# Optimization experiments

Measured on AMD Instinct MI355X. Metric: run time of the kernel, lower is better.

## Reference

```python
import jax, jax.numpy as jnp
import numpy as np

B, N, C, H, EXP = 8, 1024, 256, 8, 4
D = C // H
F = int(C * EXP * 2 / 3)  # 682, GLU hidden size
EPS = 1e-3  # keras LayerNormalization default


def layer_norm(x, g, b):
    m = jnp.mean(x, axis=-1, keepdims=True)
    v = jnp.mean(jnp.square(x - m), axis=-1, keepdims=True)
    return (x - m) * jax.lax.rsqrt(v + EPS) * g + b


def setup_inputs() -> dict:
    key = jax.random.key(0)
    ks = jax.random.split(key, 16)
    inputs = jax.random.normal(ks[0], (B, N, C), jnp.float32)
    # ragged padding mask: random valid lengths per batch element
    lengths = jax.random.randint(ks[1], (B,), N // 2, N + 1)
    valid = jnp.arange(N)[None, :] < lengths[:, None]          # [B,N]
    mask = valid[:, :, None] & valid[:, None, :]               # [B,N,N]
    interaction = jax.random.normal(ks[2], (B, N, N, H), jnp.float32)
    s = lambda k, sh, fan: jax.random.normal(k, sh, jnp.float32) / np.sqrt(fan)
    return {
        "inputs": inputs, "mask": mask, "interaction": interaction,
        "Wqkv": s(ks[3], (C, 3 * C), C), "bqkv": jnp.zeros((3 * C,), jnp.float32),
        "Wt1": s(ks[4], (H, H), H), "bt1": jnp.zeros((H,), jnp.float32),
        "Wt2": s(ks[5], (H, H), H), "bt2": jnp.zeros((H,), jnp.float32),
        "Wout": s(ks[6], (C, C), C), "bout": jnp.zeros((C,), jnp.float32),
        "ln1_g": jnp.ones((C,), jnp.float32), "ln1_b": jnp.zeros((C,), jnp.float32),
        "ln2_g": jnp.ones((C,), jnp.float32), "ln2_b": jnp.zeros((C,), jnp.float32),
        "gamma1": jnp.full((C,), 1e-5, jnp.float32),
        "gamma2": jnp.full((C,), 1e-5, jnp.float32),
        "W_wide": s(ks[7], (C, F), C), "W_gate": s(ks[8], (C, F), C),
        "W_down": s(ks[9], (F, C), F),
        "lnf_g": jnp.ones((F,), jnp.float32), "lnf_b": jnp.zeros((F,), jnp.float32),
    }


def reference(inputs, mask, interaction, Wqkv, bqkv, Wt1, bt1, Wt2, bt2,
              Wout, bout, ln1_g, ln1_b, ln2_g, ln2_b, gamma1, gamma2,
              W_wide, W_gate, W_down, lnf_g, lnf_b):
    # --- pre-norm talking-heads self-attention ---
    h = layer_norm(inputs, ln1_g, ln1_b)
    qkv = (h @ Wqkv + bqkv).reshape(B, N, 3, H, D)
    qkv = jnp.transpose(qkv, (2, 0, 3, 1, 4))                 # [3,B,H,N,D]
    q, k, v = qkv[0], qkv[1], qkv[2]
    scores = jnp.einsum('bhnd,bhmd->bhnm', q, k) / np.sqrt(D) # [B,H,N,N]
    # talking heads 1 (pre-softmax head mixing, with bias)
    scores = jnp.einsum('bhnm,hg->bgnm', scores, Wt1) + bt1[None, :, None, None]
    scores = scores + jnp.transpose(interaction, (0, 3, 1, 2))
    # keras Softmax(mask): add -1e9 to masked positions
    scores = jnp.where(mask[:, None, :, :], scores, scores - 1e9)
    attn = jax.nn.softmax(scores, axis=-1)                    # pure attention
    # talking heads 2 (post-softmax head mixing)
    attn2 = jnp.einsum('bhnm,hg->bgnm', attn, Wt2) + bt2[None, :, None, None]
    out = jnp.einsum('bhnm,bhmd->bhnd', attn2, v)
    out = jnp.transpose(out, (0, 2, 1, 3)).reshape(B, N, C)
    out = out @ Wout + bout
    x = inputs + gamma1 * out                                  # LayerScale residual
    # --- GLU FFN with inner LayerNorm ---
    h2 = layer_norm(x, ln2_g, ln2_b)
    f = jax.nn.gelu(h2 @ W_wide, approximate=False) * (h2 @ W_gate)
    f = layer_norm(f, lnf_g, lnf_b)
    f = f @ W_down
    x = x + gamma2 * f
    return x
```

## Files before the change

kernel.cpp:

```cpp
#include <hip/hip_runtime.h>
#include <hip/hip_bf16.h>
#include <math.h>

#define B_ 8
#define N_ 1024
#define C_ 256
#define H_ 8
#define D_ 32
#define F_ 682
#define FP_ 704
#define EPS_ 1e-3f

typedef const __hip_bfloat16* bf16cp;
typedef __hip_bfloat16 bf16;
typedef __attribute__((ext_vector_type(8))) short short8;
typedef __attribute__((ext_vector_type(4))) float f32x4;

__device__ __forceinline__ float b2f(bf16 v){ return __bfloat162float(v); }
__device__ __forceinline__ float us2f(unsigned int u){ return __uint_as_float(u << 16); }
__device__ __forceinline__ unsigned short f2bu(float f){
  unsigned int u = __float_as_uint(f);
  return (unsigned short)((u + 0x7FFFu + ((u >> 16) & 1u)) >> 16);
}

__device__ __forceinline__ float ldf(const void* p, size_t i, int bf){
  return bf ? b2f(((bf16cp)p)[i]) : ((const float*)p)[i];
}

struct Ptrs { const void* p[22]; };

__global__ void k_sniff(Ptrs ptrs, int* flags){
  if (threadIdx.x != 0 || blockIdx.x != 0) return;
  const int sizes[22] = {2097152, 8388608, 8388608, 196608, 768, 64, 8, 64, 8,
                         65536, 256, 256, 256, 256, 256, 256, 256,
                         174592, 174592, 174592, 682, 682};
  for (int i = 0; i < 22; i++){
    if (i == 1){ flags[i] = 0; continue; }
    const unsigned short* u = (const unsigned short*)ptrs.p[i];
    int nu = sizes[i] < 64 ? sizes[i] : 64;
    int badB = 0, badF = 0, evenAllZero = 1, oddAny = 0;
    for (int j = 0; j < nu; j++){
      unsigned short x = u[j];
      float vb = us2f((unsigned int)x);
      float ab = fabsf(vb);
      if (!(vb == 0.0f) && (!(ab <= 1e3f) || ab < 1e-30f || vb != vb)) badB++;
      if ((j & 1) == 0){ if (x) evenAllZero = 0; }
      else            { if (x) oddAny = 1; }
    }
    for (int j = 0; j + 1 < nu; j += 2){
      unsigned int w = ((unsigned int)u[j]) | (((unsigned int)u[j+1]) << 16);
      float vf = __uint_as_float(w);
      float af = fabsf(vf);
      if (!(vf == 0.0f) && (!(af <= 1e3f) || af < 1e-30f || vf != vf)) badF++;
    }
    int bf;
    if (badB > badF) bf = 0;
    else if (badF > badB) bf = 1;
    else bf = (evenAllZero && oddAny) ? 0 : 1;
    flags[i] = bf;
  }
}

__global__ __launch_bounds__(256) void k_lengths(const unsigned char* mask, int* lengths){
  __shared__ int red[256];
  int b = blockIdx.x, t = threadIdx.x;
  unsigned char c0 = mask[0], c1 = mask[1];
  int mode;
  if (c0 == 0x80u) mode = 2;
  else if (c0 == 0u) mode = 3;
  else mode = (c1 != 0u) ? 0 : 1;
  int cnt = 0;
  for (int n = t; n < N_; n += 256){
    size_t idx = ((size_t)b*N_ + n)*N_ + n;
    int v;
    if (mode == 0)      v = (mask[idx] != 0);
    else if (mode == 1) v = (((const int*)mask)[idx] != 0);
    else if (mode == 2) v = (((const unsigned short*)mask)[idx] != 0);
    else                v = (((const float*)mask)[idx] != 0.0f);
    cnt += v;
  }
  red[t] = cnt; __syncthreads();
  for (int s = 128; s > 0; s >>= 1){ if (t < s) red[t] += red[t+s]; __syncthreads(); }
  if (t == 0) lengths[b] = red[0];
}

__global__ __launch_bounds__(256) void k_ln(const void* in, const int* flags, int in_mode,
                                            const void* g, int gi, const void* bia, int bi,
                                            void* out, int out_bf16, int Clen, int stride){
  __shared__ float red[256];
  int fin = (in_mode >= 0) ? flags[in_mode] : (in_mode == -2 ? 1 : 0);
  int fg = flags[gi], fb = flags[bi];
  int row = blockIdx.x, t = threadIdx.x;
  size_t base = (size_t)row * stride;
  float xs[3];
  int nv = (Clen + 255) >> 8;
  float s = 0.f;
  for (int i = 0; i < nv; i++){
    int c = t + (i << 8);
    float v = 0.f;
    if (c < Clen) v = ldf(in, base+c, fin);
    xs[i] = v; s += v;
  }
  red[t] = s; __syncthreads();
  for (int st = 128; st > 0; st >>= 1){ if (t < st) red[t] += red[t+st]; __syncthreads(); }
  float mean = red[0] / (float)Clen; __syncthreads();
  float s2 = 0.f;
  for (int i = 0; i < nv; i++){
    int c = t + (i << 8);
    if (c < Clen){ float d = xs[i] - mean; s2 += d*d; }
  }
  red[t] = s2; __syncthreads();
  for (int st = 128; st > 0; st >>= 1){ if (t < st) red[t] += red[t+st]; __syncthreads(); }
  float rstd = rsqrtf(red[0] / (float)Clen + EPS_);
  for (int i = 0; i < nv; i++){
    int c = t + (i << 8);
    if (c < Clen){
      float v = (xs[i]-mean)*rstd*ldf(g,c,fg) + ldf(bia,c,fb);
      if (out_bf16) ((bf16*)out)[base+c] = __float2bfloat16(v);
      else          ((float*)out)[base+c] = v;
    }
  }
}

__global__ __launch_bounds__(256) void k_prepw(Ptrs ptrs, const int* flags,
                                               unsigned short* wqkvT, unsigned short* woutT,
                                               unsigned short* wwideT, unsigned short* wgateT,
                                               unsigned short* wdownT){
  __shared__ unsigned short tile[32][33];
  int which = blockIdx.y;
  const void* src; unsigned short* dst; int f, Ksrc, Nsrc, Np, Kp;
  switch (which){
    case 0:  src = ptrs.p[3];  f = flags[3];  Ksrc = 256; Nsrc = 768; Np = 768; Kp = 256; dst = wqkvT; break;
    case 1:  src = ptrs.p[9];  f = flags[9];  Ksrc = 256; Nsrc = 256; Np = 256; Kp = 256; dst = woutT; break;
    case 2:  src = ptrs.p[17]; f = flags[17]; Ksrc = 256; Nsrc = F_;  Np = FP_; Kp = 256; dst = wwideT; break;
    case 3:  src = ptrs.p[18]; f = flags[18]; Ksrc = 256; Nsrc = F_;  Np = FP_; Kp = 256; dst = wgateT; break;
    default: src = ptrs.p[19]; f = flags[19]; Ksrc = F_;  Nsrc = 256; Np = 256; Kp = FP_; dst = wdownT; break;
  }
  int tilesN = (Np + 31) >> 5, tilesK = (Kp + 31) >> 5;
  int tid = blockIdx.x;
  if (tid >= tilesN * tilesK) return;
  int tn = tid % tilesN, tk = tid / tilesN;
  int n0 = tn << 5, k0 = tk << 5;
  int tx = threadIdx.x & 31, ty = threadIdx.x >> 5;
  #pragma unroll
  for (int i = 0; i < 4; i++){
    int k = k0 + ty + i*8, n = n0 + tx;
    float v = (k < Ksrc && n < Nsrc) ? ldf(src, (size_t)k*Nsrc + n, f) : 0.f;
    tile[ty + i*8][tx] = f2bu(v);
  }
  __syncthreads();
  #pragma unroll
  for (int i = 0; i < 4; i++){
    int n = n0 + ty + i*8, k = k0 + tx;
    if (n < Np && k < Kp) dst[(size_t)n*Kp + k] = tile[tx][ty + i*8];
  }
}

__device__ __forceinline__ void gemm128_core(const unsigned short* A, const unsigned short* BT,
                                             int K, int m0, int n0,
                                             unsigned short* As, unsigned short* Bs,
                                             f32x4 (&acc)[4][4]){
  int t = threadIdx.x;
  int lane = t & 63, w = t >> 6, wr = w >> 1, wc = w & 1;
  int cl = lane & 15, cq = lane >> 4;
  int r0 = t >> 2, o0 = (t & 3) << 3;
  const unsigned short* Ap = A + (size_t)(m0 + r0) * K + o0;
  const unsigned short* Bp = BT + (size_t)(n0 + r0) * K + o0;
  for (int k0 = 0; k0 < K; k0 += 32){
    short8 a0 = *(const short8*)(Ap + k0);
    short8 a1 = *(const short8*)(Ap + (size_t)64*K + k0);
    short8 b0 = *(const short8*)(Bp + k0);
    short8 b1 = *(const short8*)(Bp + (size_t)64*K + k0);
    __syncthreads();
    *(short8*)(As + r0*40 + o0)      = a0;
    *(short8*)(As + (r0+64)*40 + o0) = a1;
    *(short8*)(Bs + r0*40 + o0)      = b0;
    *(short8*)(Bs + (r0+64)*40 + o0) = b1;
    __syncthreads();
    short8 af[4], bfr[4];
    #pragma unroll
    for (int i = 0; i < 4; i++){
      af[i]  = *(const short8*)(As + (wr*64 + i*16 + cl)*40 + cq*8);
      bfr[i] = *(const short8*)(Bs + (wc*64 + i*16 + cl)*40 + cq*8);
    }
    #pragma unroll
    for (int i = 0; i < 4; i++)
      #pragma unroll
      for (int j = 0; j < 4; j++)
        acc[i][j] = __builtin_amdgcn_mfma_f32_16x16x32_bf16(af[i], bfr[j], acc[i][j], 0, 0, 0);
  }
}

__global__ __launch_bounds__(256) void k_qkv(const bf16* Abuf, const unsigned short* WT,
                                             const void* bias, const int* flags,
                                             bf16* qb, bf16* kb, bf16* vb){
  __shared__ unsigned short As[128*40], Bs[128*40];
  int fb = flags[4];
  int m0 = blockIdx.x * 128, n0 = blockIdx.y * 128;
  f32x4 acc[4][4];
  #pragma unroll
  for (int i = 0; i < 4; i++)
    #pragma unroll
    for (int j = 0; j < 4; j++){ f32x4 z = {0.f,0.f,0.f,0.f}; acc[i][j] = z; }
  gemm128_core((const unsigned short*)Abuf, WT, C_, m0, n0, As, Bs, acc);
  int t = threadIdx.x, lane = t & 63, w = t >> 6, wr = w >> 1, wc = w & 1;
  int cl = lane & 15, cq = lane >> 4;
  #pragma unroll
  for (int j = 0; j < 4; j++){
    int n = n0 + wc*64 + j*16 + cl;
    float bv = ldf(bias, n, fb);
    int three = n >> 8, hh = (n >> 5) & 7, d = n & 31;
    bf16* dst = (three == 0) ? qb : ((three == 1) ? kb : vb);
    #pragma unroll
    for (int i = 0; i < 4; i++){
      #pragma unroll
      for (int r = 0; r < 4; r++){
        int m = m0 + wr*64 + i*16 + cq*4 + r;
        int bb = m >> 10, nn = m & 1023;
        dst[(((size_t)bb*H_ + hh)*N_ + nn)*D_ + d] = __float2bfloat16(acc[i][j][r] + bv);
      }
    }
  }
}

__global__ __launch_bounds__(256) void k_outproj(const bf16* Abuf, const unsigned short* WT,
                                                 const void* bias, const void* inputs,
                                                 const void* gamma1, const int* flags, float* xout){
  __shared__ unsigned short As[128*40], Bs[128*40];
  int fb = flags[10], fin = flags[0], fg = flags[15];
  int m0 = blockIdx.x * 128, n0 = blockIdx.y * 128;
  f32x4 acc[4][4];
  #pragma unroll
  for (int i = 0; i < 4; i++)
    #pragma unroll
    for (int j = 0; j < 4; j++){ f32x4 z = {0.f,0.f,0.f,0.f}; acc[i][j] = z; }
  gemm128_core((const unsigned short*)Abuf, WT, C_, m0, n0, As, Bs, acc);
  int t = threadIdx.x, lane = t & 63, w = t >> 6, wr = w >> 1, wc = w & 1;
  int cl = lane & 15, cq = lane >> 4;
  #pragma unroll
  for (int j = 0; j < 4; j++){
    int n = n0 + wc*64 + j*16 + cl;
    float bv = ldf(bias, n, fb);
    float gv = ldf(gamma1, n, fg);
    #pragma unroll
    for (int i = 0; i < 4; i++){
      #pragma unroll
      for (int r = 0; r < 4; r++){
        int m = m0 + wr*64 + i*16 + cq*4 + r;
        size_t idx = (size_t)m*C_ + n;
        xout[idx] = ldf(inputs, idx, fin) + gv * (acc[i][j][r] + bv);
      }
    }
  }
}

__device__ __forceinline__ float gelu_exact(float x){
  return 0.5f * x * (1.0f + erff(x * 0.70710678118654752f));
}

__global__ __launch_bounds__(256) void k_ffn1(const bf16* Abuf, const unsigned short* WwT,
                                              const unsigned short* WgT, bf16* fout){
  __shared__ unsigned short As[128*40], Bw[64*40], Bg[64*40];
  int m0 = blockIdx.x * 128, n0 = blockIdx.y * 64;
  int t = threadIdx.x, lane = t & 63, w = t >> 6, wr = w >> 1, wc = w & 1;
  int cl = lane & 15, cq = lane >> 4;
  int r0 = t >> 2, o0 = (t & 3) << 3;
  const unsigned short* A = (const unsigned short*)Abuf;
  f32x4 acc1[4][2], acc2[4][2];
  #pragma unroll
  for (int i = 0; i < 4; i++)
    #pragma unroll
    for (int j = 0; j < 2; j++){ f32x4 z = {0.f,0.f,0.f,0.f}; acc1[i][j] = z; acc2[i][j] = z; }
  const unsigned short* Ap = A + (size_t)(m0 + r0) * C_ + o0;
  const unsigned short* Bwp = WwT + (size_t)(n0 + r0) * C_ + o0;
  const unsigned short* Bgp = WgT + (size_t)(n0 + r0) * C_ + o0;
  for (int k0 = 0; k0 < C_; k0 += 32){
    short8 a0 = *(const short8*)(Ap + k0);
    short8 a1 = *(const short8*)(Ap + (size_t)64*C_ + k0);
    short8 b0, c0;
    if (r0 < 64){
      b0 = *(const short8*)(Bwp + k0);
      c0 = *(const short8*)(Bgp + k0);
    }
    __syncthreads();
    *(short8*)(As + r0*40 + o0)      = a0;
    *(short8*)(As + (r0+64)*40 + o0) = a1;
    if (r0 < 64){
      *(short8*)(Bw + r0*40 + o0) = b0;
      *(short8*)(Bg + r0*40 + o0) = c0;
    }
    __syncthreads();
    short8 af[4], bfr[2], cfr[2];
    #pragma unroll
    for (int i = 0; i < 4; i++)
      af[i] = *(const short8*)(As + (wr*64 + i*16 + cl)*40 + cq*8);
    #pragma unroll
    for (int j = 0; j < 2; j++){
      bfr[j] = *(const short8*)(Bw + (wc*32 + j*16 + cl)*40 + cq*8);
      cfr[j] = *(const short8*)(Bg + (wc*32 + j*16 + cl)*40 + cq*8);
    }
    #pragma unroll
    for (int i = 0; i < 4; i++)
      #pragma unroll
      for (int j = 0; j < 2; j++){
        acc1[i][j] = __builtin_amdgcn_mfma_f32_16x16x32_bf16(af[i], bfr[j], acc1[i][j], 0, 0, 0);
        acc2[i][j] = __builtin_amdgcn_mfma_f32_16x16x32_bf16(af[i], cfr[j], acc2[i][j], 0, 0, 0);
      }
  }
  #pragma unroll
  for (int j = 0; j < 2; j++){
    int n = n0 + wc*32 + j*16 + cl;
    #pragma unroll
    for (int i = 0; i < 4; i++){
      #pragma unroll
      for (int r = 0; r < 4; r++){
        int m = m0 + wr*64 + i*16 + cq*4 + r;
        float v = (n < F_) ? gelu_exact(acc1[i][j][r]) * acc2[i][j][r] : 0.f;
        fout[(size_t)m*FP_ + n] = __float2bfloat16(v);
      }
    }
  }
}

__global__ __launch_bounds__(256) void k_down(const bf16* Abuf, const unsigned short* WT,
                                              const float* xbuf, const void* gamma2,
                                              const int* flags, void* out){
  __shared__ unsigned short As[128*40], Bs[128*40];
  int fg = flags[16], fo = flags[0];
  int m0 = blockIdx.x * 128, n0 = blockIdx.y * 128;
  f32x4 acc[4][4];
  #pragma unroll
  for (int i = 0; i < 4; i++)
    #pragma unroll
    for (int j = 0; j < 4; j++){ f32x4 z = {0.f,0.f,0.f,0.f}; acc[i][j] = z; }
  gemm128_core((const unsigned short*)Abuf, WT, FP_, m0, n0, As, Bs, acc);
  int t = threadIdx.x, lane = t & 63, w = t >> 6, wr = w >> 1, wc = w & 1;
  int cl = lane & 15, cq = lane >> 4;
  #pragma unroll
  for (int j = 0; j < 4; j++){
    int n = n0 + wc*64 + j*16 + cl;
    float gv = ldf(gamma2, n, fg);
    #pragma unroll
    for (int i = 0; i < 4; i++){
      #pragma unroll
      for (int r = 0; r < 4; r++){
        int m = m0 + wr*64 + i*16 + cq*4 + r;
        size_t idx = (size_t)m*C_ + n;
        float val = xbuf[idx] + gv * acc[i][j][r];
        if (fo) ((bf16*)out)[idx] = __float2bfloat16(val);
        else    ((float*)out)[idx] = val;
      }
    }
  }
}

__global__ __launch_bounds__(256) void k_vsum(const bf16* vb, float* vsum){
  __shared__ float red[8][32];
  int bg = blockIdx.x;
  int t = threadIdx.x;
  int d = t & 31, mg = t >> 5;
  float s = 0.f;
  for (int m = mg*128; m < mg*128 + 128; m++)
    s += b2f(vb[((size_t)bg*N_ + m)*D_ + d]);
  red[mg][d] = s; __syncthreads();
  if (t < 32){
    float a = 0.f;
    #pragma unroll
    for (int i = 0; i < 8; i++) a += red[i][t];
    vsum[(size_t)bg*D_ + t] = a;
  }
}

__global__ __launch_bounds__(256) void k_stats2(const bf16* qb, const bf16* kb,
                                                const void* Wt1, const void* bt1, const void* inter,
                                                const int* flags, const int* lengths, float2* stats){
  __shared__ float w1s[64], b1v[8];
  __shared__ float swM[4][8][16], swL[4][8][16];
  int fw1 = flags[5], fb1 = flags[6], fint = flags[2];
  int t = threadIdx.x;
  int ntile = blockIdx.x, b = blockIdx.y;
  int n0 = ntile * 16;
  int len = lengths[b];
  if (t < 64) w1s[t] = ldf(Wt1, t, fw1) * 0.17677669529663687f;
  if (t < 8)  b1v[t] = ldf(bt1, t, fb1);
  __syncthreads();
  int lane = t & 63, w = t >> 6;
  int c = lane & 15, q = lane >> 4;
  const unsigned short* qus = (const unsigned short*)qb;
  const unsigned short* kus = (const unsigned short*)kb;
  short8 qfrag[8];
  #pragma unroll
  for (int h = 0; h < 8; h++)
    qfrag[h] = *(const short8*)(qus + (((size_t)b*8 + h)*N_ + n0 + c)*D_ + q*8);
  int n_g = n0 + c;
  float M[8], L[8];
  #pragma unroll
  for (int g = 0; g < 8; g++){ M[g] = -1e30f; L[g] = 0.f; }

  for (int ci = 0; ci < 8; ci++){
    int m0c = w*256 + ci*32;
    #pragma unroll
    for (int mt = 0; mt < 2; mt++){
      int m0t = m0c + mt*16;
      f32x4 sfr[8];
      #pragma unroll
      for (int h = 0; h < 8; h++){
        short8 kf = *(const short8*)(kus + (((size_t)b*8 + h)*N_ + m0t + c)*D_ + q*8);
        f32x4 z = {0.f,0.f,0.f,0.f};
        sfr[h] = __builtin_amdgcn_mfma_f32_16x16x32_bf16(kf, qfrag[h], z, 0, 0, 0);
      }
      float ifl[4][8];
      #pragma unroll
      for (int r = 0; r < 4; r++){
        int m = m0t + q*4 + r;
        size_t i8 = ((size_t)b*N_ + n_g)*N_ + m;
        if (fint){
          uint4 iv = *(const uint4*)((const unsigned short*)inter + i8*8);
          ifl[r][0]=us2f(iv.x&0xffffu); ifl[r][1]=us2f(iv.x>>16);
          ifl[r][2]=us2f(iv.y&0xffffu); ifl[r][3]=us2f(iv.y>>16);
          ifl[r][4]=us2f(iv.z&0xffffu); ifl[r][5]=us2f(iv.z>>16);
          ifl[r][6]=us2f(iv.w&0xffffu); ifl[r][7]=us2f(iv.w>>16);
        } else {
          const float* fp = (const float*)inter + i8*8;
          #pragma unroll
          for (int g = 0; g < 8; g++) ifl[r][g] = fp[g];
        }
      }
      #pragma unroll
      for (int g = 0; g < 8; g++){
        float sv[4];
        #pragma unroll
        for (int r = 0; r < 4; r++){
          int m = m0t + q*4 + r;
          float v = b1v[g] + ifl[r][g];
          #pragma unroll
          for (int h = 0; h < 8; h++) v += sfr[h][r] * w1s[h*8 + g];
          bool ok = (n_g >= len) || (m < len);
          sv[r] = ok ? v : -1e30f;
        }
        float tmax = fmaxf(fmaxf(sv[0], sv[1]), fmaxf(sv[2], sv[3]));
        float Mn = fmaxf(M[g], tmax);
        float f = __expf(M[g] - Mn);
        L[g] = L[g]*f + __expf(sv[0]-Mn) + __expf(sv[1]-Mn) + __expf(sv[2]-Mn) + __expf(sv[3]-Mn);
        M[g] = Mn;
      }
    }
  }
  #pragma unroll
  for (int g = 0; g < 8; g++){
    #pragma unroll
    for (int sft = 16; sft <= 32; sft <<= 1){
      float Mo = __shfl_xor(M[g], sft);
      float Lo = __shfl_xor(L[g], sft);
      float Mn = fmaxf(M[g], Mo);
      L[g] = L[g]*__expf(M[g]-Mn) + Lo*__expf(Mo-Mn);
      M[g] = Mn;
    }
  }
  if (lane < 16){
    #pragma unroll
    for (int g = 0; g < 8; g++){ swM[w][g][c] = M[g]; swL[w][g][c] = L[g]; }
  }
  __syncthreads();
  if (t < 128){
    int g = t >> 4, nl = t & 15;
    float Mf = fmaxf(fmaxf(swM[0][g][nl], swM[1][g][nl]), fmaxf(swM[2][g][nl], swM[3][g][nl]));
    float Lf = 0.f;
    #pragma unroll
    for (int wv = 0; wv < 4; wv++) Lf += swL[wv][g][nl] * __expf(swM[wv][g][nl] - Mf);
    stats[((size_t)b*8 + g)*N_ + n0 + nl] = make_float2(Mf, Lf);
  }
}

__global__ __launch_bounds__(256) void k_attn2(const bf16* qb, const bf16* kb, const bf16* vb,
                                               const void* Wt1, const void* bt1,
                                               const void* Wt2, const void* bt2,
                                               const void* inter, const int* flags,
                                               const int* lengths, const float2* stats,
                                               const float* vsum, bf16* aobuf){
  __shared__ unsigned short a2s[4][8][640];
  __shared__ unsigned short vts[4][1280];
  __shared__ float w1s[64], w2s[64], b1v[8], b2v[8];
  __shared__ float moff[8][16];
  __shared__ float vsumS[8][32];
  __shared__ float osum[4][528];
  int fw1 = flags[5], fb1 = flags[6], fw2 = flags[7], fb2 = flags[8], fint = flags[2];
  int t = threadIdx.x;
  int ntile = blockIdx.x, b = blockIdx.y;
  int n0 = ntile * 16;
  int len = lengths[b];
  if (t < 64){ w1s[t] = ldf(Wt1, t, fw1) * 0.17677669529663687f; w2s[t] = ldf(Wt2, t, fw2); }
  if (t < 8){ b1v[t] = ldf(bt1, t, fb1); b2v[t] = ldf(bt2, t, fb2); }
  if (t < 128){
    int g = t >> 4, nl = t & 15;
    float2 st = stats[((size_t)b*8 + g)*N_ + n0 + nl];
    moff[g][nl] = st.x + __logf(st.y);
  }
  {
    int g = t >> 5, d = t & 31;
    vsumS[g][d] = vsum[((size_t)b*8 + g)*D_ + d];
  }
  __syncthreads();
  int lane = t & 63, w = t >> 6;
  int c = lane & 15, q = lane >> 4;
  const unsigned short* qus = (const unsigned short*)qb;
  const unsigned short* kus = (const unsigned short*)kb;
  const unsigned short* vus = (const unsigned short*)vb;
  short8 qfrag[8];
  #pragma unroll
  for (int h = 0; h < 8; h++)
    qfrag[h] = *(const short8*)(qus + (((size_t)b*8 + h)*N_ + n0 + c)*D_ + q*8);
  float moffreg[8][4];
  #pragma unroll
  for (int g = 0; g < 8; g++)
    #pragma unroll
    for (int r = 0; r < 4; r++) moffreg[g][r] = moff[g][q*4 + r];
  f32x4 acc[8][2];
  #pragma unroll
  for (int gg = 0; gg < 8; gg++){ f32x4 z = {0.f,0.f,0.f,0.f}; acc[gg][0] = z; acc[gg][1] = z; }

  for (int ci = 0; ci < 8; ci++){
    int m0c = w*256 + ci*32;
    #pragma unroll
    for (int mt = 0; mt < 2; mt++){
      int m0t = m0c + mt*16;
      f32x4 sfr[8];
      #pragma unroll
      for (int h = 0; h < 8; h++){
        short8 kf = *(const short8*)(kus + (((size_t)b*8 + h)*N_ + m0t + c)*D_ + q*8);
        f32x4 z = {0.f,0.f,0.f,0.f};
        sfr[h] = __builtin_amdgcn_mfma_f32_16x16x32_bf16(qfrag[h], kf, z, 0, 0, 0);
      }
      int m_g = m0t + c;
      bool mok = (m_g < len);
      #pragma unroll
      for (int r = 0; r < 4; r++){
        int n_l = q*4 + r, n_gg = n0 + n_l;
        size_t i8 = ((size_t)b*N_ + n_gg)*N_ + m_g;
        float ifl[8];
        if (fint){
          uint4 iv = *(const uint4*)((const unsigned short*)inter + i8*8);
          ifl[0]=us2f(iv.x&0xffffu); ifl[1]=us2f(iv.x>>16);
          ifl[2]=us2f(iv.y&0xffffu); ifl[3]=us2f(iv.y>>16);
          ifl[4]=us2f(iv.z&0xffffu); ifl[5]=us2f(iv.z>>16);
          ifl[6]=us2f(iv.w&0xffffu); ifl[7]=us2f(iv.w>>16);
        } else {
          const float* fp = (const float*)inter + i8*8;
          #pragma unroll
          for (int g = 0; g < 8; g++) ifl[g] = fp[g];
        }
        bool ok = (n_gg >= len) || mok;
        float p[8];
        #pragma unroll
        for (int g = 0; g < 8; g++){
          float v = b1v[g] + ifl[g];
          #pragma unroll
          for (int h = 0; h < 8; h++) v += sfr[h][r] * w1s[h*8 + g];
          v = ok ? v : -1e30f;
          p[g] = __expf(v - moffreg[g][r]);
        }
        #pragma unroll
        for (int gg = 0; gg < 8; gg++){
          float a2 = 0.f;
          #pragma unroll
          for (int g = 0; g < 8; g++) a2 += p[g] * w2s[g*8 + gg];
          a2s[w][gg][n_l*40 + mt*16 + c] = f2bu(a2);
        }
      }
    }
    #pragma unroll
    for (int gg = 0; gg < 8; gg++){
      short8 v0 = *(const short8*)(vus + (((size_t)b*8 + gg)*N_ + m0c + c)*D_ + q*8);
      short8 v1 = *(const short8*)(vus + (((size_t)b*8 + gg)*N_ + m0c + 16 + c)*D_ + q*8);
      #pragma unroll
      for (int j = 0; j < 8; j++){
        vts[w][(q*8 + j)*40 + c]      = (unsigned short)v0[j];
        vts[w][(q*8 + j)*40 + 16 + c] = (unsigned short)v1[j];
      }
      short8 af  = *(const short8*)&a2s[w][gg][c*40 + q*8];
      short8 bf0 = *(const short8*)&vts[w][c*40 + q*8];
      short8 bf1 = *(const short8*)&vts[w][(16 + c)*40 + q*8];
      acc[gg][0] = __builtin_amdgcn_mfma_f32_16x16x32_bf16(af, bf0, acc[gg][0], 0, 0, 0);
      acc[gg][1] = __builtin_amdgcn_mfma_f32_16x16x32_bf16(af, bf1, acc[gg][1], 0, 0, 0);
    }
  }
  for (int gg = 0; gg < 8; gg++){
    #pragma unroll
    for (int dt = 0; dt < 2; dt++)
      #pragma unroll
      for (int r = 0; r < 4; r++)
        osum[w][(q*4 + r)*33 + dt*16 + c] = acc[gg][dt][r];
    __syncthreads();
    #pragma unroll
    for (int e = t; e < 512; e += 256){
      int nl = e >> 5, d = e & 31;
      float val = osum[0][nl*33 + d] + osum[1][nl*33 + d]
                + osum[2][nl*33 + d] + osum[3][nl*33 + d]
                + b2v[gg] * vsumS[gg][d];
      aobuf[((size_t)b*N_ + n0 + nl)*C_ + gg*D_ + d] = __float2bfloat16(val);
    }
    __syncthreads();
  }
}

extern "C" void kernel_launch(void* const* d_in, const int* in_sizes, int n_in,
                              void* d_out, int out_size, void* d_ws, size_t ws_size,
                              hipStream_t stream) {
  Ptrs ptrs;
  for (int i = 0; i < 22; i++) ptrs.p[i] = d_in[i];
  const unsigned char* mask = (const unsigned char*)d_in[1];

  char* ws = (char*)d_ws;
  size_t o = 0;
  size_t o_flags = o; o += 256;
  size_t o_len   = o; o += 256;
  size_t o_stats = o; o += (size_t)B_*H_*N_*sizeof(float2);
  size_t o_vsum  = o; o += (size_t)B_*H_*D_*4;
  size_t o_h     = o; o += (size_t)B_*N_*C_*2;
  size_t o_q     = o; o += (size_t)B_*N_*C_*2;
  size_t o_k     = o; o += (size_t)B_*N_*C_*2;
  size_t o_v     = o; o += (size_t)B_*N_*C_*2;
  size_t o_ao    = o; o += (size_t)B_*N_*C_*2;
  size_t o_x     = o; o += (size_t)B_*N_*C_*4;
  size_t o_f     = o; o += (size_t)B_*N_*FP_*2;
  size_t o_wq    = o; o += (size_t)768*256*2;
  size_t o_wo    = o; o += (size_t)256*256*2;
  size_t o_ww    = o; o += (size_t)FP_*256*2;
  size_t o_wg    = o; o += (size_t)FP_*256*2;
  size_t o_wd    = o; o += (size_t)256*FP_*2;

  int*    flags   = (int*)(ws + o_flags);
  int*    lengths = (int*)(ws + o_len);
  float2* stats   = (float2*)(ws + o_stats);
  float*  vsum    = (float*)(ws + o_vsum);
  bf16*   hbuf    = (bf16*)(ws + o_h);
  bf16*   qbuf    = (bf16*)(ws + o_q);
  bf16*   kbuf    = (bf16*)(ws + o_k);
  bf16*   vbuf    = (bf16*)(ws + o_v);
  bf16*   aobuf   = (bf16*)(ws + o_ao);
  float*  xbuf    = (float*)(ws + o_x);
  bf16*   fbuf    = (bf16*)(ws + o_f);
  unsigned short* wqkvT  = (unsigned short*)(ws + o_wq);
  unsigned short* woutT  = (unsigned short*)(ws + o_wo);
  unsigned short* wwideT = (unsigned short*)(ws + o_ww);
  unsigned short* wgateT = (unsigned short*)(ws + o_wg);
  unsigned short* wdownT = (unsigned short*)(ws + o_wd);

  k_sniff<<<1, 64, 0, stream>>>(ptrs, flags);
  k_prepw<<<dim3(192, 5), 256, 0, stream>>>(ptrs, flags, wqkvT, woutT, wwideT, wgateT, wdownT);
  k_lengths<<<8, 256, 0, stream>>>(mask, lengths);
  k_ln<<<B_*N_, 256, 0, stream>>>(d_in[0], flags, 0, d_in[11], 11, d_in[12], 12, hbuf, 1, C_, C_);
  k_qkv<<<dim3(64, 6), 256, 0, stream>>>(hbuf, wqkvT, d_in[4], flags, qbuf, kbuf, vbuf);
  k_vsum<<<64, 256, 0, stream>>>(vbuf, vsum);
  k_stats2<<<dim3(64, 8), 256, 0, stream>>>(qbuf, kbuf, d_in[5], d_in[6], d_in[2],
                                            flags, lengths, stats);
  k_attn2<<<dim3(64, 8), 256, 0, stream>>>(qbuf, kbuf, vbuf, d_in[5], d_in[6], d_in[7], d_in[8],
                                           d_in[2], flags, lengths, stats, vsum, aobuf);
  k_outproj<<<dim3(64, 2), 256, 0, stream>>>(aobuf, woutT, d_in[10], d_in[0], d_in[15], flags, xbuf);
  k_ln<<<B_*N_, 256, 0, stream>>>(xbuf, flags, -1, d_in[13], 13, d_in[14], 14, hbuf, 1, C_, C_);
  k_ffn1<<<dim3(64, 11), 256, 0, stream>>>(hbuf, wwideT, wgateT, fbuf);
  k_ln<<<B_*N_, 256, 0, stream>>>(fbuf, flags, -2, d_in[20], 20, d_in[21], 21, fbuf, 1, F_, FP_);
  k_down<<<dim3(64, 2), 256, 0, stream>>>(fbuf, wdownT, xbuf, d_in[16], flags, d_out);
}
```

Measured before the change: 1.024 ms.

## Materialize unnormalized softmax probabilities once and split attention into two passes

The attention is restructured so scores and the interaction tensor are computed only once. Pass A computes the exponentiated scores without max-subtraction, writes them as a bf16 probability buffer of B*H*N*N, and accumulates row sums. Pass B reads that buffer, normalizes it, applies the post-softmax head mix, and multiplies by a pre-transposed V, with heads split over a z grid dimension. This removes the duplicated QK and interaction reads from the old stats-then-attn pair but adds a large 128MB intermediate round trip, and dropping max-subtraction risks exp overflow. The format sniff kernel is also parallelized across blocks with wave ballots.

```diff
diff --git a/kernel.cpp b/kernel.cpp
--- a/kernel.cpp
+++ b/kernel.cpp
@@ -29,30 +29,40 @@
 
 struct Ptrs { const void* p[22]; };
 
-__global__ void k_sniff(Ptrs ptrs, int* flags){
-  if (threadIdx.x != 0 || blockIdx.x != 0) return;
+__global__ __launch_bounds__(64) void k_sniffp(Ptrs ptrs, int* flags){
+  int i = blockIdx.x;
+  int lane = threadIdx.x;
+  if (i == 1){ if (lane == 0) flags[1] = 0; return; }
   const int sizes[22] = {2097152, 8388608, 8388608, 196608, 768, 64, 8, 64, 8,
                          65536, 256, 256, 256, 256, 256, 256, 256,
                          174592, 174592, 174592, 682, 682};
-  for (int i = 0; i < 22; i++){
-    if (i == 1){ flags[i] = 0; continue; }
-    const unsigned short* u = (const unsigned short*)ptrs.p[i];
-    int nu = sizes[i] < 64 ? sizes[i] : 64;
-    int badB = 0, badF = 0, evenAllZero = 1, oddAny = 0;
-    for (int j = 0; j < nu; j++){
-      unsigned short x = u[j];
-      float vb = us2f((unsigned int)x);
-      float ab = fabsf(vb);
-      if (!(vb == 0.0f) && (!(ab <= 1e3f) || ab < 1e-30f || vb != vb)) badB++;
-      if ((j & 1) == 0){ if (x) evenAllZero = 0; }
-      else            { if (x) oddAny = 1; }
-    }
-    for (int j = 0; j + 1 < nu; j += 2){
-      unsigned int w = ((unsigned int)u[j]) | (((unsigned int)u[j+1]) << 16);
-      float vf = __uint_as_float(w);
-      float af = fabsf(vf);
-      if (!(vf == 0.0f) && (!(af <= 1e3f) || af < 1e-30f || vf != vf)) badF++;
-    }
+  const unsigned short* u = (const unsigned short*)ptrs.p[i];
+  int nu = sizes[i] < 64 ? sizes[i] : 64;
+  unsigned short x = 0;
+  if (lane < nu) x = u[lane];
+  int predB = 0;
+  if (lane < nu){
+    float vb = us2f((unsigned int)x);
+    float ab = fabsf(vb);
+    predB = (!(vb == 0.0f) && (!(ab <= 1e3f) || ab < 1e-30f || vb != vb)) ? 1 : 0;
+  }
+  unsigned long long mB = __ballot(predB);
+  int badB = __popcll(mB);
+  unsigned long long mEven = __ballot(lane < nu && (lane & 1) == 0 && x != 0);
+  unsigned long long mOdd  = __ballot(lane < nu && (lane & 1) == 1 && x != 0);
+  int evenAllZero = (mEven == 0ull);
+  int oddAny = (mOdd != 0ull);
+  unsigned short xa = (unsigned short)__shfl((int)x, (lane * 2) & 63);
+  unsigned short xb = (unsigned short)__shfl((int)x, (lane * 2 + 1) & 63);
+  int predF = 0;
+  if (lane < (nu >> 1)){
+    unsigned int w = ((unsigned int)xa) | (((unsigned int)xb) << 16);
+    float vf = __uint_as_float(w);
+    float af = fabsf(vf);
+    predF = (!(vf == 0.0f) && (!(af <= 1e3f) || af < 1e-30f || vf != vf)) ? 1 : 0;
+  }
+  int badF = __popcll(__ballot(predF));
+  if (lane == 0){
     int bf;
     if (badB > badF) bf = 0;
     else if (badF > badB) bf = 1;
@@ -153,6 +163,24 @@
   for (int i = 0; i < 4; i++){
     int n = n0 + ty + i*8, k = k0 + tx;
     if (n < Np && k < Kp) dst[(size_t)n*Kp + k] = tile[tx][ty + i*8];
+  }
+}
+
+__global__ __launch_bounds__(256) void k_vt(const bf16* vb, unsigned short* vt){
+  __shared__ unsigned short tile[32][34];
+  int mt = blockIdx.x, bg = blockIdx.y;
+  int tx = threadIdx.x & 31, ty = threadIdx.x >> 5;
+  const unsigned short* vus = (const unsigned short*)vb;
+  #pragma unroll
+  for (int i = 0; i < 4; i++){
+    int m = mt*32 + ty + i*8;
+    tile[ty + i*8][tx] = vus[((size_t)bg*N_ + m)*D_ + tx];
+  }
+  __syncthreads();
+  #pragma unroll
+  for (int i = 0; i < 4; i++){
+    int d = ty + i*8;
+    vt[((size_t)bg*D_ + d)*N_ + mt*32 + tx] = tile[tx][d];
   }
 }
 
@@ -371,14 +399,16 @@
   }
 }
 
-__global__ __launch_bounds__(256) void k_stats2(const bf16* qb, const bf16* kb,
-                                                const void* Wt1, const void* bt1, const void* inter,
-                                                const int* flags, const int* lengths, float2* stats){
+__global__ __launch_bounds__(256) void k_passA(const bf16* qb, const bf16* kb,
+                                               const void* Wt1, const void* bt1, const void* inter,
+                                               const int* flags, const int* lengths,
+                                               unsigned short* P, float* Lp){
   __shared__ float w1s[64], b1v[8];
-  __shared__ float swM[4][8][16], swL[4][8][16];
+  __shared__ unsigned short ps[4][8][640];
+  __shared__ float swL[4][8][16];
   int fw1 = flags[5], fb1 = flags[6], fint = flags[2];
   int t = threadIdx.x;
-  int ntile = blockIdx.x, b = blockIdx.y;
+  int ntile = blockIdx.x, b = blockIdx.y, z = blockIdx.z;
   int n0 = ntile * 16;
   int len = lengths[b];
   if (t < 64) w1s[t] = ldf(Wt1, t, fw1) * 0.17677669529663687f;
@@ -392,13 +422,14 @@
   #pragma unroll
   for (int h = 0; h < 8; h++)
     qfrag[h] = *(const short8*)(qus + (((size_t)b*8 + h)*N_ + n0 + c)*D_ + q*8);
-  int n_g = n0 + c;
-  float M[8], L[8];
-  #pragma unroll
-  for (int g = 0; g < 8; g++){ M[g] = -1e30f; L[g] = 0.f; }
-
-  for (int ci = 0; ci < 8; ci++){
-    int m0c = w*256 + ci*32;
+  float Lacc[8][4];
+  #pragma unroll
+  for (int g = 0; g < 8; g++)
+    #pragma unroll
+    for (int r = 0; r < 4; r++) Lacc[g][r] = 0.f;
+
+  for (int ci = 0; ci < 4; ci++){
+    int m0c = z*512 + w*128 + ci*32;
     #pragma unroll
     for (int mt = 0; mt < 2; mt++){
       int m0t = m0c + mt*16;
@@ -406,130 +437,8 @@
       #pragma unroll
       for (int h = 0; h < 8; h++){
         short8 kf = *(const short8*)(kus + (((size_t)b*8 + h)*N_ + m0t + c)*D_ + q*8);
-        f32x4 z = {0.f,0.f,0.f,0.f};
-        sfr[h] = __builtin_amdgcn_mfma_f32_16x16x32_bf16(kf, qfrag[h], z, 0, 0, 0);
-      }
-      float ifl[4][8];
-      #pragma unroll
-      for (int r = 0; r < 4; r++){
-        int m = m0t + q*4 + r;
-        size_t i8 = ((size_t)b*N_ + n_g)*N_ + m;
-        if (fint){
-          uint4 iv = *(const uint4*)((const unsigned short*)inter + i8*8);
-          ifl[r][0]=us2f(iv.x&0xffffu); ifl[r][1]=us2f(iv.x>>16);
-          ifl[r][2]=us2f(iv.y&0xffffu); ifl[r][3]=us2f(iv.y>>16);
-          ifl[r][4]=us2f(iv.z&0xffffu); ifl[r][5]=us2f(iv.z>>16);
-          ifl[r][6]=us2f(iv.w&0xffffu); ifl[r][7]=us2f(iv.w>>16);
-        } else {
-          const float* fp = (const float*)inter + i8*8;
-          #pragma unroll
-          for (int g = 0; g < 8; g++) ifl[r][g] = fp[g];
-        }
-      }
-      #pragma unroll
-      for (int g = 0; g < 8; g++){
-        float sv[4];
-        #pragma unroll
-        for (int r = 0; r < 4; r++){
-          int m = m0t + q*4 + r;
-          float v = b1v[g] + ifl[r][g];
-          #pragma unroll
-          for (int h = 0; h < 8; h++) v += sfr[h][r] * w1s[h*8 + g];
-          bool ok = (n_g >= len) || (m < len);
-          sv[r] = ok ? v : -1e30f;
-        }
-        float tmax = fmaxf(fmaxf(sv[0], sv[1]), fmaxf(sv[2], sv[3]));
-        float Mn = fmaxf(M[g], tmax);
-        float f = __expf(M[g] - Mn);
-        L[g] = L[g]*f + __expf(sv[0]-Mn) + __expf(sv[1]-Mn) + __expf(sv[2]-Mn) + __expf(sv[3]-Mn);
-        M[g] = Mn;
-      }
-    }
-  }
-  #pragma unroll
-  for (int g = 0; g < 8; g++){
-    #pragma unroll
-    for (int sft = 16; sft <= 32; sft <<= 1){
-      float Mo = __shfl_xor(M[g], sft);
-      float Lo = __shfl_xor(L[g], sft);
-      float Mn = fmaxf(M[g], Mo);
-      L[g] = L[g]*__expf(M[g]-Mn) + Lo*__expf(Mo-Mn);
-      M[g] = Mn;
-    }
-  }
-  if (lane < 16){
-    #pragma unroll
-    for (int g = 0; g < 8; g++){ swM[w][g][c] = M[g]; swL[w][g][c] = L[g]; }
-  }
-  __syncthreads();
-  if (t < 128){
-    int g = t >> 4, nl = t & 15;
-    float Mf = fmaxf(fmaxf(swM[0][g][nl], swM[1][g][nl]), fmaxf(swM[2][g][nl], swM[3][g][nl]));
-    float Lf = 0.f;
-    #pragma unroll
-    for (int wv = 0; wv < 4; wv++) Lf += swL[wv][g][nl] * __expf(swM[wv][g][nl] - Mf);
-    stats[((size_t)b*8 + g)*N_ + n0 + nl] = make_float2(Mf, Lf);
-  }
-}
-
-__global__ __launch_bounds__(256) void k_attn2(const bf16* qb, const bf16* kb, const bf16* vb,
-                                               const void* Wt1, const void* bt1,
-                                               const void* Wt2, const void* bt2,
-                                               const void* inter, const int* flags,
-                                               const int* lengths, const float2* stats,
-                                               const float* vsum, bf16* aobuf){
-  __shared__ unsigned short a2s[4][8][640];
-  __shared__ unsigned short vts[4][1280];
-  __shared__ float w1s[64], w2s[64], b1v[8], b2v[8];
-  __shared__ float moff[8][16];
-  __shared__ float vsumS[8][32];
-  __shared__ float osum[4][528];
-  int fw1 = flags[5], fb1 = flags[6], fw2 = flags[7], fb2 = flags[8], fint = flags[2];
-  int t = threadIdx.x;
-  int ntile = blockIdx.x, b = blockIdx.y;
-  int n0 = ntile * 16;
-  int len = lengths[b];
-  if (t < 64){ w1s[t] = ldf(Wt1, t, fw1) * 0.17677669529663687f; w2s[t] = ldf(Wt2, t, fw2); }
-  if (t < 8){ b1v[t] = ldf(bt1, t, fb1); b2v[t] = ldf(bt2, t, fb2); }
-  if (t < 128){
-    int g = t >> 4, nl = t & 15;
-    float2 st = stats[((size_t)b*8 + g)*N_ + n0 + nl];
-    moff[g][nl] = st.x + __logf(st.y);
-  }
-  {
-    int g = t >> 5, d = t & 31;
-    vsumS[g][d] = vsum[((size_t)b*8 + g)*D_ + d];
-  }
-  __syncthreads();
-  int lane = t & 63, w = t >> 6;
-  int c = lane & 15, q = lane >> 4;
-  const unsigned short* qus = (const unsigned short*)qb;
-  const unsigned short* kus = (const unsigned short*)kb;
-  const unsigned short* vus = (const unsigned short*)vb;
-  short8 qfrag[8];
-  #pragma unroll
-  for (int h = 0; h < 8; h++)
-    qfrag[h] = *(const short8*)(qus + (((size_t)b*8 + h)*N_ + n0 + c)*D_ + q*8);
-  float moffreg[8][4];
-  #pragma unroll
-  for (int g = 0; g < 8; g++)
-    #pragma unroll
-    for (int r = 0; r < 4; r++) moffreg[g][r] = moff[g][q*4 + r];
-  f32x4 acc[8][2];
-  #pragma unroll
-  for (int gg = 0; gg < 8; gg++){ f32x4 z = {0.f,0.f,0.f,0.f}; acc[gg][0] = z; acc[gg][1] = z; }
-
-  for (int ci = 0; ci < 8; ci++){
-    int m0c = w*256 + ci*32;
-    #pragma unroll
-    for (int mt = 0; mt < 2; mt++){
-      int m0t = m0c + mt*16;
-      f32x4 sfr[8];
-      #pragma unroll
-      for (int h = 0; h < 8; h++){
-        short8 kf = *(const short8*)(kus + (((size_t)b*8 + h)*N_ + m0t + c)*D_ + q*8);
-        f32x4 z = {0.f,0.f,0.f,0.f};
-        sfr[h] = __builtin_amdgcn_mfma_f32_16x16x32_bf16(qfrag[h], kf, z, 0, 0, 0);
+        f32x4 zz = {0.f,0.f,0.f,0.f};
+        sfr[h] = __builtin_amdgcn_mfma_f32_16x16x32_bf16(qfrag[h], kf, zz, 0, 0, 0);
       }
       int m_g = m0t + c;
       bool mok = (m_g < len);
@@ -550,54 +459,136 @@
           for (int g = 0; g < 8; g++) ifl[g] = fp[g];
         }
         bool ok = (n_gg >= len) || mok;
-        float p[8];
         #pragma unroll
         for (int g = 0; g < 8; g++){
           float v = b1v[g] + ifl[g];
           #pragma unroll
           for (int h = 0; h < 8; h++) v += sfr[h][r] * w1s[h*8 + g];
-          v = ok ? v : -1e30f;
-          p[g] = __expf(v - moffreg[g][r]);
+          float e = ok ? __expf(v) : 0.f;
+          Lacc[g][r] += e;
+          ps[w][g][n_l*40 + mt*16 + c] = f2bu(e);
         }
-        #pragma unroll
-        for (int gg = 0; gg < 8; gg++){
-          float a2 = 0.f;
-          #pragma unroll
-          for (int g = 0; g < 8; g++) a2 += p[g] * w2s[g*8 + gg];
-          a2s[w][gg][n_l*40 + mt*16 + c] = f2bu(a2);
-        }
-      }
-    }
-    #pragma unroll
-    for (int gg = 0; gg < 8; gg++){
-      short8 v0 = *(const short8*)(vus + (((size_t)b*8 + gg)*N_ + m0c + c)*D_ + q*8);
-      short8 v1 = *(const short8*)(vus + (((size_t)b*8 + gg)*N_ + m0c + 16 + c)*D_ + q*8);
-      #pragma unroll
-      for (int j = 0; j < 8; j++){
-        vts[w][(q*8 + j)*40 + c]      = (unsigned short)v0[j];
-        vts[w][(q*8 + j)*40 + 16 + c] = (unsigned short)v1[j];
-      }
-      short8 af  = *(const short8*)&a2s[w][gg][c*40 + q*8];
-      short8 bf0 = *(const short8*)&vts[w][c*40 + q*8];
-      short8 bf1 = *(const short8*)&vts[w][(16 + c)*40 + q*8];
+      }
+    }
+    #pragma unroll
+    for (int it = 0; it < 8; it++){
+      int row = it*16 + (lane >> 2);
+      int g = row >> 4, n = row & 15, chunk = lane & 3;
+      short8 pv = *(const short8*)&ps[w][g][n*40 + chunk*8];
+      *(short8*)(P + (((size_t)b*8 + g)*N_ + n0 + n)*N_ + m0c + chunk*8) = pv;
+    }
+  }
+  #pragma unroll
+  for (int g = 0; g < 8; g++)
+    #pragma unroll
+    for (int r = 0; r < 4; r++){
+      float v = Lacc[g][r];
+      v += __shfl_xor(v, 1); v += __shfl_xor(v, 2);
+      v += __shfl_xor(v, 4); v += __shfl_xor(v, 8);
+      Lacc[g][r] = v;
+    }
+  if (c == 0){
+    #pragma unroll
+    for (int g = 0; g < 8; g++)
+      #pragma unroll
+      for (int r = 0; r < 4; r++) swL[w][g][q*4 + r] = Lacc[g][r];
+  }
+  __syncthreads();
+  if (t < 128){
+    int g = t >> 4, nl = t & 15;
+    float Lf = swL[0][g][nl] + swL[1][g][nl] + swL[2][g][nl] + swL[3][g][nl];
+    Lp[(((size_t)b*8 + g)*N_ + n0 + nl)*2 + z] = Lf;
+  }
+}
+
+__global__ __launch_bounds__(256) void k_passB(const unsigned short* P, const unsigned short* vt,
+                                               const void* Wt2, const void* bt2,
+                                               const int* flags, const float* Lp,
+                                               const float* vsum, bf16* aobuf){
+  __shared__ float w2s[64], b2v[8];
+  __shared__ float rLs[8][16];
+  __shared__ float vsumS[4][32];
+  __shared__ float osum[4][528];
+  int fw2 = flags[7], fb2 = flags[8];
+  int t = threadIdx.x;
+  int ntile = blockIdx.x, b = blockIdx.y, zh = blockIdx.z;
+  int n0 = ntile * 16;
+  if (t < 64) w2s[t] = ldf(Wt2, t, fw2);
+  if (t < 8)  b2v[t] = ldf(bt2, t, fb2);
+  if (t < 128){
+    int g = t >> 4, nl = t & 15;
+    const float* lp = Lp + (((size_t)b*8 + g)*N_ + n0 + nl)*2;
+    rLs[g][nl] = 1.0f / (lp[0] + lp[1]);
+  }
+  if (t >= 128 && t < 256){
+    int e = t - 128;
+    int g2 = e >> 5, d = e & 31;
+    vsumS[g2][d] = vsum[((size_t)b*8 + zh*4 + g2)*D_ + d];
+  }
+  __syncthreads();
+  int lane = t & 63, w = t >> 6;
+  int c = lane & 15, q = lane >> 4;
+  float rL[8];
+  #pragma unroll
+  for (int g = 0; g < 8; g++) rL[g] = rLs[g][c];
+  float w2r[8][4];
+  #pragma unroll
+  for (int g = 0; g < 8; g++)
+    #pragma unroll
+    for (int j = 0; j < 4; j++) w2r[g][j] = w2s[g*8 + zh*4 + j];
+  f32x4 acc[4][2];
+  #pragma unroll
+  for (int gg = 0; gg < 4; gg++){ f32x4 z = {0.f,0.f,0.f,0.f}; acc[gg][0] = z; acc[gg][1] = z; }
+
+  for (int ci = 0; ci < 8; ci++){
+    int m0c = w*256 + ci*32;
+    short8 pf[8];
+    #pragma unroll
+    for (int g = 0; g < 8; g++)
+      pf[g] = *(const short8*)(P + (((size_t)b*8 + g)*N_ + n0 + c)*N_ + m0c + q*8);
+    float a2[4][8];
+    #pragma unroll
+    for (int gg = 0; gg < 4; gg++)
+      #pragma unroll
+      for (int j = 0; j < 8; j++) a2[gg][j] = 0.f;
+    #pragma unroll
+    for (int j = 0; j < 8; j++){
+      #pragma unroll
+      for (int g = 0; g < 8; g++){
+        float png = us2f((unsigned int)(unsigned short)pf[g][j]) * rL[g];
+        a2[0][j] += png * w2r[g][0];
+        a2[1][j] += png * w2r[g][1];
+        a2[2][j] += png * w2r[g][2];
+        a2[3][j] += png * w2r[g][3];
+      }
+    }
+    #pragma unroll
+    for (int gg = 0; gg < 4; gg++){
+      short8 af;
+      #pragma unroll
+      for (int j = 0; j < 8; j++) af[j] = (short)f2bu(a2[gg][j]);
+      int ggg = zh*4 + gg;
+      short8 bf0 = *(const short8*)(vt + (((size_t)b*8 + ggg)*D_ + c)*N_ + m0c + q*8);
+      short8 bf1 = *(const short8*)(vt + (((size_t)b*8 + ggg)*D_ + 16 + c)*N_ + m0c + q*8);
       acc[gg][0] = __builtin_amdgcn_mfma_f32_16x16x32_bf16(af, bf0, acc[gg][0], 0, 0, 0);
       acc[gg][1] = __builtin_amdgcn_mfma_f32_16x16x32_bf16(af, bf1, acc[gg][1], 0, 0, 0);
     }
   }
-  for (int gg = 0; gg < 8; gg++){
+  for (int gg = 0; gg < 4; gg++){
     #pragma unroll
     for (int dt = 0; dt < 2; dt++)
       #pragma unroll
       for (int r = 0; r < 4; r++)
         osum[w][(q*4 + r)*33 + dt*16 + c] = acc[gg][dt][r];
     __syncthreads();
+    int ggg = zh*4 + gg;
     #pragma unroll
     for (int e = t; e < 512; e += 256){
       int nl = e >> 5, d = e & 31;
       float val = osum[0][nl*33 + d] + osum[1][nl*33 + d]
                 + osum[2][nl*33 + d] + osum[3][nl*33 + d]
-                + b2v[gg] * vsumS[gg][d];
-      aobuf[((size_t)b*N_ + n0 + nl)*C_ + gg*D_ + d] = __float2bfloat16(val);
+                + b2v[ggg] * vsumS[gg][d];
+      aobuf[((size_t)b*N_ + n0 + nl)*C_ + ggg*D_ + d] = __float2bfloat16(val);
     }
     __syncthreads();
   }
@@ -614,12 +605,13 @@
   size_t o = 0;
   size_t o_flags = o; o += 256;
   size_t o_len   = o; o += 256;
-  size_t o_stats = o; o += (size_t)B_*H_*N_*sizeof(float2);
+  size_t o_L     = o; o += (size_t)B_*H_*N_*2*4;
   size_t o_vsum  = o; o += (size_t)B_*H_*D_*4;
   size_t o_h     = o; o += (size_t)B_*N_*C_*2;
   size_t o_q     = o; o += (size_t)B_*N_*C_*2;
   size_t o_k     = o; o += (size_t)B_*N_*C_*2;
   size_t o_v     = o; o += (size_t)B_*N_*C_*2;
+  size_t o_vt    = o; o += (size_t)B_*N_*C_*2;
   size_t o_ao    = o; o += (size_t)B_*N_*C_*2;
   size_t o_x     = o; o += (size_t)B_*N_*C_*4;
   size_t o_f     = o; o += (size_t)B_*N_*FP_*2;
@@ -628,15 +620,17 @@
   size_t o_ww    = o; o += (size_t)FP_*256*2;
   size_t o_wg    = o; o += (size_t)FP_*256*2;
   size_t o_wd    = o; o += (size_t)256*FP_*2;
+  size_t o_P     = o; o += (size_t)B_*H_*N_*N_*2;
 
   int*    flags   = (int*)(ws + o_flags);
   int*    lengths = (int*)(ws + o_len);
-  float2* stats   = (float2*)(ws + o_stats);
+  float*  Lp      = (float*)(ws + o_L);
   float*  vsum    = (float*)(ws + o_vsum);
   bf16*   hbuf    = (bf16*)(ws + o_h);
   bf16*   qbuf    = (bf16*)(ws + o_q);
   bf16*   kbuf    = (bf16*)(ws + o_k);
   bf16*   vbuf    = (bf16*)(ws + o_v);
+  unsigned short* vtbuf = (unsigned short*)(ws + o_vt);
   bf16*   aobuf   = (bf16*)(ws + o_ao);
   float*  xbuf    = (float*)(ws + o_x);
   bf16*   fbuf    = (bf16*)(ws + o_f);
@@ -645,17 +639,19 @@
   unsigned short* wwideT = (unsigned short*)(ws + o_ww);
   unsigned short* wgateT = (unsigned short*)(ws + o_wg);
   unsigned short* wdownT = (unsigned short*)(ws + o_wd);
-
-  k_sniff<<<1, 64, 0, stream>>>(ptrs, flags);
+  unsigned short* Pbuf   = (unsigned short*)(ws + o_P);
+
+  k_sniffp<<<22, 64, 0, stream>>>(ptrs, flags);
   k_prepw<<<dim3(192, 5), 256, 0, stream>>>(ptrs, flags, wqkvT, woutT, wwideT, wgateT, wdownT);
   k_lengths<<<8, 256, 0, stream>>>(mask, lengths);
   k_ln<<<B_*N_, 256, 0, stream>>>(d_in[0], flags, 0, d_in[11], 11, d_in[12], 12, hbuf, 1, C_, C_);
   k_qkv<<<dim3(64, 6), 256, 0, stream>>>(hbuf, wqkvT, d_in[4], flags, qbuf, kbuf, vbuf);
+  k_vt<<<dim3(32, 64), 256, 0, stream>>>(vbuf, vtbuf);
   k_vsum<<<64, 256, 0, stream>>>(vbuf, vsum);
-  k_stats2<<<dim3(64, 8), 256, 0, stream>>>(qbuf, kbuf, d_in[5], d_in[6], d_in[2],
-                                            flags, lengths, stats);
-  k_attn2<<<dim3(64, 8), 256, 0, stream>>>(qbuf, kbuf, vbuf, d_in[5], d_in[6], d_in[7], d_in[8],
-                                           d_in[2], flags, lengths, stats, vsum, aobuf);
+  k_passA<<<dim3(64, 8, 2), 256, 0, stream>>>(qbuf, kbuf, d_in[5], d_in[6], d_in[2],
+                                              flags, lengths, Pbuf, Lp);
+  k_passB<<<dim3(64, 8, 2), 256, 0, stream>>>(Pbuf, vtbuf, d_in[7], d_in[8],
+                                              flags, Lp, vsum, aobuf);
   k_outproj<<<dim3(64, 2), 256, 0, stream>>>(aobuf, woutT, d_in[10], d_in[0], d_in[15], flags, xbuf);
   k_ln<<<B_*N_, 256, 0, stream>>>(xbuf, flags, -1, d_in[13], 13, d_in[14], 14, hbuf, 1, C_, C_);
   k_ffn1<<<dim3(64, 11), 256, 0, stream>>>(hbuf, wwideT, wgateT, fbuf);
```

Measured after the change: 851.1 us. 16.9% less time.
